# Optimization experiments

Measured on AMD Instinct MI355X. Metric: run time of the kernel, lower is better.

## Reference

```python
import jax, jax.numpy as jnp
import numpy as np

L, H, C, V, T_BLK = 12, 12, 768, 50257, 1024
D = C // H  # head dim = 64


def _layernorm(x, g, b, eps=1e-5):
    m = jnp.mean(x, axis=-1, keepdims=True)
    v = jnp.mean(jnp.square(x - m), axis=-1, keepdims=True)
    return (x - m) * jax.lax.rsqrt(v + eps) * g + b


def setup_inputs() -> dict:
    key = jax.random.key(0)
    ks = jax.random.split(key, 8)
    B, T = 8, 1024
    s = 0.02
    sp = 0.02 / np.sqrt(2 * L)  # c_proj special init
    return {
        "idx": jax.random.randint(ks[0], (B, T), 0, V, dtype=jnp.int32),
        "wte": jax.random.normal(ks[1], (V, C), jnp.float32) * s,
        "wpe": jax.random.normal(ks[2], (T_BLK, C), jnp.float32) * s,
        "ln1_g": jnp.ones((L, C), jnp.float32),
        "ln1_b": jnp.zeros((L, C), jnp.float32),
        "w_qkv": jax.random.normal(ks[3], (L, C, 3 * C), jnp.float32) * s,
        "b_qkv": jnp.zeros((L, 3 * C), jnp.float32),
        "w_ao": jax.random.normal(ks[4], (L, C, C), jnp.float32) * sp,
        "b_ao": jnp.zeros((L, C), jnp.float32),
        "ln2_g": jnp.ones((L, C), jnp.float32),
        "ln2_b": jnp.zeros((L, C), jnp.float32),
        "w_fc": jax.random.normal(ks[5], (L, C, 4 * C), jnp.float32) * s,
        "b_fc": jnp.zeros((L, 4 * C), jnp.float32),
        "w_mo": jax.random.normal(ks[6], (L, 4 * C, C), jnp.float32) * sp,
        "b_mo": jnp.zeros((L, C), jnp.float32),
        "lnf_g": jnp.ones((C,), jnp.float32),
        "lnf_b": jnp.zeros((C,), jnp.float32),
    }


def reference(idx, wte, wpe, ln1_g, ln1_b, w_qkv, b_qkv, w_ao, b_ao,
              ln2_g, ln2_b, w_fc, b_fc, w_mo, b_mo, lnf_g, lnf_b):
    B, T = idx.shape
    scale = 1.0 / np.sqrt(D)
    causal = jnp.tril(jnp.ones((T, T), dtype=bool))  # [T,T]

    x = wte[idx] + wpe[:T]  # [B,T,C]

    def block(x, p):
        g1, b1, wq, bq, wo, bo, g2, b2_, wf, bf, w2, b2m = p
        h = _layernorm(x, g1, b1)
        qkv = h @ wq + bq  # [B,T,3C]
        q, k, v = jnp.split(qkv, 3, axis=-1)
        q = q.reshape(B, T, H, D)
        k = k.reshape(B, T, H, D)
        v = v.reshape(B, T, H, D)
        att = jnp.einsum('bqhd,bkhd->bhqk', q, k) * scale
        att = jnp.where(causal, att, -jnp.inf)
        att = jax.nn.softmax(att, axis=-1)
        y = jnp.einsum('bhqk,bkhd->bqhd', att, v).reshape(B, T, C)
        x = x + y @ wo + bo
        h2 = _layernorm(x, g2, b2_)
        x = x + jax.nn.gelu(h2 @ wf + bf, approximate=False) @ w2 + b2m
        return x, None

    params = (ln1_g, ln1_b, w_qkv, b_qkv, w_ao, b_ao,
              ln2_g, ln2_b, w_fc, b_fc, w_mo, b_mo)
    x, _ = jax.lax.scan(block, x, params)

    x = _layernorm(x, lnf_g, lnf_b)
    # inference path: logits only for last position, lm_head tied to wte
    logits = x[:, -1:, :] @ wte.T  # [B,1,V]
    return logits
```

## Files before the change

kernel.cpp:

```cpp
#include <hip/hip_runtime.h>

#define B_ 8
#define T_ 1024
#define C_ 768
#define H_ 12
#define L_ 12
#define V_ 50257

typedef __bf16 bf16_t;
typedef __bf16 bf16x8 __attribute__((ext_vector_type(8)));
typedef __bf16 bf16x4 __attribute__((ext_vector_type(4)));
typedef float f32x4 __attribute__((ext_vector_type(4)));

#define AS1 __attribute__((address_space(1)))
#define AS3 __attribute__((address_space(3)))

__device__ __forceinline__ unsigned short f2bf(float f) {
  bf16_t h = (bf16_t)f;
  return __builtin_bit_cast(unsigned short, h);
}

__device__ __forceinline__ unsigned short bfbits(bf16_t h) {
  return __builtin_bit_cast(unsigned short, h);
}

template<int CTRL>
__device__ __forceinline__ float dppf(float x) {
  return __builtin_bit_cast(float, __builtin_amdgcn_update_dpp(
      0, __builtin_bit_cast(int, x), CTRL, 0xF, 0xF, true));
}
__device__ __forceinline__ float red16_max(float x) {
  x = fmaxf(x, dppf<0xB1>(x));
  x = fmaxf(x, dppf<0x4E>(x));
  x = fmaxf(x, dppf<0x124>(x));
  x = fmaxf(x, dppf<0x128>(x));
  return x;
}
__device__ __forceinline__ float red16_sum(float x) {
  x += dppf<0xB1>(x);
  x += dppf<0x4E>(x);
  x += dppf<0x124>(x);
  x += dppf<0x128>(x);
  return x;
}

__global__ __launch_bounds__(192) void embed_kernel(
    const int* __restrict__ idx, const float* __restrict__ wte,
    const float* __restrict__ wpe, float* __restrict__ xf)
{
  const int bt = blockIdx.x;
  const int t = bt & (T_ - 1);
  const int tok = idx[bt];
  const int c4 = threadIdx.x << 2;
  float4 a = *(const float4*)(wte + (size_t)tok * C_ + c4);
  float4 p = *(const float4*)(wpe + (size_t)t * C_ + c4);
  float4 r; r.x = a.x + p.x; r.y = a.y + p.y; r.z = a.z + p.z; r.w = a.w + p.w;
  *(float4*)(xf + (size_t)bt * C_ + c4) = r;
}

template<bool LAST>
__global__ __launch_bounds__(256) void ln_kernel(
    const float* __restrict__ x, const float* __restrict__ gw,
    const float* __restrict__ bw, unsigned short* __restrict__ obf,
    float* __restrict__ of)
{
  __shared__ float red[8];
  const size_t row = LAST ? ((size_t)blockIdx.x * T_ + (T_ - 1)) : (size_t)blockIdx.x;
  const float* xr = x + row * C_;
  const int t = threadIdx.x;
  float v0 = xr[t], v1 = xr[t + 256], v2 = xr[t + 512];
  float s = v0 + v1 + v2;
  #pragma unroll
  for (int off = 32; off; off >>= 1) s += __shfl_xor(s, off);
  if ((t & 63) == 0) red[t >> 6] = s;
  __syncthreads();
  const float mean = (red[0] + red[1] + red[2] + red[3]) * (1.0f / C_);
  const float d0 = v0 - mean, d1 = v1 - mean, d2 = v2 - mean;
  float ss = d0 * d0 + d1 * d1 + d2 * d2;
  #pragma unroll
  for (int off = 32; off; off >>= 1) ss += __shfl_xor(ss, off);
  if ((t & 63) == 0) red[4 + (t >> 6)] = ss;
  __syncthreads();
  const float var = (red[4] + red[5] + red[6] + red[7]) * (1.0f / C_);
  const float rs = rsqrtf(var + 1e-5f);
  float o0 = d0 * rs * gw[t] + bw[t];
  float o1 = d1 * rs * gw[t + 256] + bw[t + 256];
  float o2 = d2 * rs * gw[t + 512] + bw[t + 512];
  if (LAST) {
    float* orow = of + (size_t)blockIdx.x * C_;
    orow[t] = o0; orow[t + 256] = o1; orow[t + 512] = o2;
  } else {
    unsigned short* orow = obf + row * C_;
    orow[t] = f2bf(o0); orow[t + 256] = f2bf(o1); orow[t + 512] = f2bf(o2);
  }
}

__global__ __launch_bounds__(256) void cvtw4_kernel(
    const float* __restrict__ wq, const float* __restrict__ wa,
    const float* __restrict__ wf, const float* __restrict__ wm,
    unsigned short* __restrict__ out)
{
  __shared__ float tile[32][33];
  const int i = blockIdx.x;
  const float* W; unsigned short* Wt; int K, N, tix;
  if (i < 1728)      { W = wq; Wt = out;                 K = C_;     N = 3 * C_; tix = i; }
  else if (i < 2304) { W = wa; Wt = out + 3 * C_ * C_;   K = C_;     N = C_;     tix = i - 1728; }
  else if (i < 4608) { W = wf; Wt = out + 4 * C_ * C_;   K = C_;     N = 4 * C_; tix = i - 2304; }
  else               { W = wm; Wt = out + 8 * C_ * C_;   K = 4 * C_; N = C_;     tix = i - 4608; }
  const int ntx = N >> 5;
  const int kb = (tix / ntx) << 5, nb = (tix % ntx) << 5;
  const int t = threadIdx.x;
  {
    const int k = t >> 3, n4 = (t & 7) << 2;
    float4 v = *(const float4*)(W + (size_t)(kb + k) * N + nb + n4);
    tile[k][n4] = v.x; tile[k][n4 + 1] = v.y; tile[k][n4 + 2] = v.z; tile[k][n4 + 3] = v.w;
  }
  __syncthreads();
  {
    const int n = t >> 3, k4 = (t & 7) << 2;
    ushort4 o;
    o.x = f2bf(tile[k4][n]);     o.y = f2bf(tile[k4 + 1][n]);
    o.z = f2bf(tile[k4 + 2][n]); o.w = f2bf(tile[k4 + 3][n]);
    *(ushort4*)(Wt + (size_t)(nb + n) * K + kb + k4) = o;
  }
}

template<int EPI>
__global__ __launch_bounds__(256, 2) void gemm_bt(
    const unsigned short* __restrict__ A, const unsigned short* __restrict__ Bt,
    const float* __restrict__ bias, float* __restrict__ Cf,
    unsigned short* __restrict__ Cb, int M, int N, int K, int nx)
{
  (void)M; (void)nx;
  __shared__ unsigned short As[2][128 * 64];
  __shared__ unsigned short Bs[2][128 * 64];
  const int tid = threadIdx.x;
  const int lane = tid & 63;
  const int w = tid >> 6;
  const int wr = w >> 1, wc = w & 1;
  const int l15 = lane & 15, l4 = lane >> 4;
  const int swz = lane & 7;

  const int bid = blockIdx.x;
  const int xcd = bid & 7;
  const int j = bid >> 3;
  const int mblk = xcd * 8 + (j & 7);
  const int nblk = j >> 3;
  const int m0 = mblk * 128, n0 = nblk * 128;

  f32x4 acc[4][4] = {};

  const int srow = lane >> 3;
  const int schunk = (lane & 7) ^ srow;
  const unsigned short* aSrc = A + (size_t)(m0 + w * 32 + srow) * K + schunk * 8;
  const unsigned short* bSrc = Bt + (size_t)(n0 + w * 32 + srow) * K + schunk * 8;
  const int ldsRowBase = (w * 32) * 64;

  auto stage = [&](int kt, int p) {
    const int k0 = kt << 6;
    #pragma unroll
    for (int jj = 0; jj < 4; ++jj)
      __builtin_amdgcn_global_load_lds(
          (const AS1 unsigned int*)(aSrc + (size_t)jj * 8 * K + k0),
          (AS3 unsigned int*)(&As[p][ldsRowBase + jj * 8 * 64]), 16, 0, 0);
    #pragma unroll
    for (int jj = 0; jj < 4; ++jj)
      __builtin_amdgcn_global_load_lds(
          (const AS1 unsigned int*)(bSrc + (size_t)jj * 8 * K + k0),
          (AS3 unsigned int*)(&Bs[p][ldsRowBase + jj * 8 * 64]), 16, 0, 0);
  };

  auto compute = [&](int p) {
    const unsigned short* aw = &As[p][(wr * 64) * 64];
    const unsigned short* bw2 = &Bs[p][(wc * 64) * 64];
    #pragma unroll
    for (int ks = 0; ks < 2; ++ks) {
      bf16x8 af[4], bf[4];
      #pragma unroll
      for (int mf = 0; mf < 4; ++mf)
        af[mf] = *(const bf16x8*)(aw + (mf * 16 + l15) * 64 + (((ks << 2) | l4) ^ swz) * 8);
      #pragma unroll
      for (int nf = 0; nf < 4; ++nf)
        bf[nf] = *(const bf16x8*)(bw2 + (nf * 16 + l15) * 64 + (((ks << 2) | l4) ^ swz) * 8);
      __builtin_amdgcn_s_setprio(1);
      #pragma unroll
      for (int mf = 0; mf < 4; ++mf)
        #pragma unroll
        for (int nf = 0; nf < 4; ++nf)
          acc[mf][nf] = __builtin_amdgcn_mfma_f32_16x16x32_bf16(af[mf], bf[nf], acc[mf][nf], 0, 0, 0);
      __builtin_amdgcn_s_setprio(0);
    }
  };

  const int nk = K >> 6;
  stage(0, 0);
  for (int kt = 0; kt < nk - 1; ++kt) {
    const int p = kt & 1;
    stage(kt + 1, p ^ 1);
    asm volatile("s_waitcnt vmcnt(8)" ::: "memory");
    __builtin_amdgcn_s_barrier();
    compute(p);
    __builtin_amdgcn_s_barrier();
  }
  asm volatile("s_waitcnt vmcnt(0)" ::: "memory");
  __builtin_amdgcn_s_barrier();
  compute((nk - 1) & 1);

  #pragma unroll
  for (int mf = 0; mf < 4; ++mf) {
    #pragma unroll
    for (int nf = 0; nf < 4; ++nf) {
      const int col = n0 + wc * 64 + nf * 16 + l15;
      const float bv = bias[col];
      int hh = 0, dd = 0;
      unsigned short* qkvo = nullptr;
      if constexpr (EPI == 3) {
        const int which = col / C_;
        const int rem = col - which * C_;
        hh = rem >> 6; dd = rem & 63;
        qkvo = Cb + (size_t)which * ((size_t)B_ * H_ * T_ * 64);
      }
      #pragma unroll
      for (int i = 0; i < 4; ++i) {
        const int row = m0 + wr * 64 + mf * 16 + l4 * 4 + i;
        float v = acc[mf][nf][i] + bv;
        if constexpr (EPI == 1) {
          Cf[(size_t)row * N + col] += v;
        } else if constexpr (EPI == 2) {
          float g = 0.5f * v * (1.0f + erff(v * 0.70710678118f));
          Cb[(size_t)row * N + col] = f2bf(g);
        } else {
          const int bb = row >> 10, tt = row & (T_ - 1);
          qkvo[(((size_t)bb * H_ + hh) * T_ + tt) * 64 + dd] = f2bf(v);
        }
      }
    }
  }
}

__global__ __launch_bounds__(256) void attn_kernel(
    const unsigned short* __restrict__ Qb, const unsigned short* __restrict__ Kb,
    const unsigned short* __restrict__ Vb, unsigned short* __restrict__ y)
{
  const int pb = blockIdx.x / 96;
  const int bh = blockIdx.x % 96;
  const int h = bh % H_;
  const int b = bh / H_;
  const int tid = threadIdx.x, lane = tid & 63, w = tid >> 6;
  const int l15 = lane & 15, l4 = lane >> 4;

  const int qw = (w < 2) ? (pb * 64 + w * 32) : ((15 - pb) * 64 + (w - 2) * 32);
  const int NT = (17 - pb) >> 1;

  __shared__ unsigned short Ks[128 * 64];
  __shared__ unsigned short Vt[64 * 136];
  __shared__ unsigned short Pb[4][32 * 74];

  const unsigned short* qp = Qb + ((size_t)bh * T_ + qw) * 64;
  bf16x8 qf[2][2];
  #pragma unroll
  for (int mf = 0; mf < 2; ++mf)
    #pragma unroll
    for (int ks = 0; ks < 2; ++ks)
      qf[mf][ks] = *(const bf16x8*)(qp + (mf * 16 + l15) * 64 + ks * 32 + l4 * 8);

  f32x4 o[2][4] = {};
  float mrow[2][4], lrow[2][4];
  #pragma unroll
  for (int mf = 0; mf < 2; ++mf)
    #pragma unroll
    for (int i = 0; i < 4; ++i) { mrow[mf][i] = -1e30f; lrow[mf][i] = 0.0f; }

  const unsigned short* kb0 = Kb + (size_t)bh * T_ * 64;
  const unsigned short* vb0 = Vb + (size_t)bh * T_ * 64;
  const int ck = w;
  const int skey = lane;
  const int sw = (skey & 7);

  bf16x8 kr0, kr1, kr2, kr3, vr0, vr1, vr2, vr3;
  {
    const unsigned short* kp = kb0 + (size_t)skey * 64;
    const unsigned short* vp = vb0 + (size_t)skey * 64;
    kr0 = *(const bf16x8*)(kp + ck * 8);
    kr1 = *(const bf16x8*)(kp + (ck + 4) * 8);
    kr2 = *(const bf16x8*)(kp + 64 * 64 + ck * 8);
    kr3 = *(const bf16x8*)(kp + 64 * 64 + (ck + 4) * 8);
    vr0 = *(const bf16x8*)(vp + ck * 8);
    vr1 = *(const bf16x8*)(vp + (ck + 4) * 8);
    vr2 = *(const bf16x8*)(vp + 64 * 64 + ck * 8);
    vr3 = *(const bf16x8*)(vp + 64 * 64 + (ck + 4) * 8);
  }

  for (int kt = 0; kt < NT; ++kt) {
    const int k0 = kt << 7;
    __syncthreads();
    *(bf16x8*)(Ks + skey * 64 + ((ck ^ sw) * 8)) = kr0;
    *(bf16x8*)(Ks + skey * 64 + (((ck + 4) ^ sw) * 8)) = kr1;
    *(bf16x8*)(Ks + (skey + 64) * 64 + ((ck ^ sw) * 8)) = kr2;
    *(bf16x8*)(Ks + (skey + 64) * 64 + (((ck + 4) ^ sw) * 8)) = kr3;
    #pragma unroll
    for (int jj = 0; jj < 8; ++jj) {
      Vt[(ck * 8 + jj) * 136 + skey]            = bfbits(vr0[jj]);
      Vt[((ck + 4) * 8 + jj) * 136 + skey]      = bfbits(vr1[jj]);
      Vt[(ck * 8 + jj) * 136 + skey + 64]       = bfbits(vr2[jj]);
      Vt[((ck + 4) * 8 + jj) * 136 + skey + 64] = bfbits(vr3[jj]);
    }
    __syncthreads();
    if (kt + 1 < NT) {
      const int kn = (kt + 1) << 7;
      const unsigned short* kp = kb0 + (size_t)(kn + skey) * 64;
      const unsigned short* vp = vb0 + (size_t)(kn + skey) * 64;
      kr0 = *(const bf16x8*)(kp + ck * 8);
      kr1 = *(const bf16x8*)(kp + (ck + 4) * 8);
      kr2 = *(const bf16x8*)(kp + 64 * 64 + ck * 8);
      kr3 = *(const bf16x8*)(kp + 64 * 64 + (ck + 4) * 8);
      vr0 = *(const bf16x8*)(vp + ck * 8);
      vr1 = *(const bf16x8*)(vp + (ck + 4) * 8);
      vr2 = *(const bf16x8*)(vp + 64 * 64 + ck * 8);
      vr3 = *(const bf16x8*)(vp + 64 * 64 + (ck + 4) * 8);
    }

    #pragma unroll
    for (int h2 = 0; h2 < 2; ++h2) {
      const int kh0 = k0 + h2 * 64;
      if (kh0 > qw + 31) continue;

      f32x4 s[2][4] = {};
      __builtin_amdgcn_s_setprio(1);
      #pragma unroll
      for (int ks = 0; ks < 2; ++ks) {
        #pragma unroll
        for (int nfk = 0; nfk < 4; ++nfk) {
          const int key = h2 * 64 + nfk * 16 + l15;
          bf16x8 kf = *(const bf16x8*)(Ks + key * 64 + ((((ks << 2) | l4) ^ (l15 & 7)) * 8));
          #pragma unroll
          for (int mf = 0; mf < 2; ++mf)
            s[mf][nfk] = __builtin_amdgcn_mfma_f32_16x16x32_bf16(qf[mf][ks], kf, s[mf][nfk], 0, 0, 0);
        }
      }
      __builtin_amdgcn_s_setprio(0);

      #pragma unroll
      for (int mf = 0; mf < 2; ++mf) {
        const int qrow = qw + mf * 16 + l4 * 4;
        const bool fullt = (kh0 + 63) <= (qw + mf * 16);
        float pvv[4][4], tm[4];
        #pragma unroll
        for (int i = 0; i < 4; ++i) {
          const int q = qrow + i;
          float m_ = -1e30f;
          #pragma unroll
          for (int nfk = 0; nfk < 4; ++nfk) {
            float x = s[mf][nfk][i] * 0.125f;
            x = fullt ? x : ((kh0 + nfk * 16 + l15 <= q) ? x : -1e30f);
            pvv[nfk][i] = x;
            m_ = fmaxf(m_, x);
          }
          tm[i] = red16_max(m_);
        }
        bool need = false;
        #pragma unroll
        for (int i = 0; i < 4; ++i) need |= (tm[i] > mrow[mf][i] + 8.0f);
        if (__any(need)) {
          #pragma unroll
          for (int i = 0; i < 4; ++i) {
            const float mnew = fmaxf(mrow[mf][i], tm[i]);
            const float alpha = __expf(mrow[mf][i] - mnew);
            mrow[mf][i] = mnew;
            lrow[mf][i] *= alpha;
            #pragma unroll
            for (int nf = 0; nf < 4; ++nf) o[mf][nf][i] *= alpha;
          }
        }
        #pragma unroll
        for (int i = 0; i < 4; ++i) {
          float rsum = 0.0f;
          #pragma unroll
          for (int nfk = 0; nfk < 4; ++nfk) {
            const float p = __expf(pvv[nfk][i] - mrow[mf][i]);
            pvv[nfk][i] = p; rsum += p;
          }
          rsum = red16_sum(rsum);
          lrow[mf][i] += rsum;
        }
        #pragma unroll
        for (int nfk = 0; nfk < 4; ++nfk)
          #pragma unroll
          for (int i = 0; i < 4; ++i)
            Pb[w][(mf * 16 + l4 * 4 + i) * 74 + nfk * 16 + l15] = f2bf(pvv[nfk][i]);
      }

      bf16x8 pa[2][2];
      #pragma unroll
      for (int mf = 0; mf < 2; ++mf)
        #pragma unroll
        for (int k2 = 0; k2 < 2; ++k2)
          pa[mf][k2] = *(const bf16x8*)(Pb[w] + (mf * 16 + l15) * 74 + k2 * 32 + l4 * 8);
      __builtin_amdgcn_s_setprio(1);
      #pragma unroll
      for (int nf = 0; nf < 4; ++nf) {
        const int d = nf * 16 + l15;
        #pragma unroll
        for (int k2 = 0; k2 < 2; ++k2) {
          bf16x8 vf = *(const bf16x8*)(Vt + d * 136 + h2 * 64 + k2 * 32 + l4 * 8);
          #pragma unroll
          for (int mf = 0; mf < 2; ++mf)
            o[mf][nf] = __builtin_amdgcn_mfma_f32_16x16x32_bf16(pa[mf][k2], vf, o[mf][nf], 0, 0, 0);
        }
      }
      __builtin_amdgcn_s_setprio(0);
    }
  }

  #pragma unroll
  for (int mf = 0; mf < 2; ++mf) {
    #pragma unroll
    for (int i = 0; i < 4; ++i) {
      const float inv = 1.0f / lrow[mf][i];
      const int q = qw + mf * 16 + l4 * 4 + i;
      unsigned short* yr = y + (size_t)(b * T_ + q) * C_ + h * 64;
      #pragma unroll
      for (int nf = 0; nf < 4; ++nf)
        yr[nf * 16 + l15] = f2bf(o[mf][nf][i] * inv);
    }
  }
}

__global__ __launch_bounds__(256) void head_kernel(
    const float* __restrict__ lnf, const float* __restrict__ wte,
    float* __restrict__ out)
{
  __shared__ float xs[B_ * C_];
  for (int i = threadIdx.x; i < B_ * C_; i += 256) xs[i] = lnf[i];
  __syncthreads();
  const int w = threadIdx.x >> 6, lane = threadIdx.x & 63;
  const int v = blockIdx.x * 4 + w;
  if (v >= V_) return;
  const float* wv = wte + (size_t)v * C_ + lane * 12;
  float4 w0 = *(const float4*)(wv);
  float4 w1 = *(const float4*)(wv + 4);
  float4 w2 = *(const float4*)(wv + 8);
  float acc[B_];
  #pragma unroll
  for (int bb = 0; bb < B_; ++bb) {
    const float* xr = xs + bb * C_ + lane * 12;
    float4 x0 = *(const float4*)(xr);
    float4 x1 = *(const float4*)(xr + 4);
    float4 x2 = *(const float4*)(xr + 8);
    acc[bb] = w0.x * x0.x + w0.y * x0.y + w0.z * x0.z + w0.w * x0.w
            + w1.x * x1.x + w1.y * x1.y + w1.z * x1.z + w1.w * x1.w
            + w2.x * x2.x + w2.y * x2.y + w2.z * x2.z + w2.w * x2.w;
  }
  #pragma unroll
  for (int off = 32; off; off >>= 1) {
    #pragma unroll
    for (int bb = 0; bb < B_; ++bb)
      acc[bb] += __shfl_xor(acc[bb], off);
  }
  if (lane == 0) {
    #pragma unroll
    for (int bb = 0; bb < B_; ++bb)
      out[(size_t)bb * V_ + v] = acc[bb];
  }
}

extern "C" void kernel_launch(void* const* d_in, const int* in_sizes, int n_in,
                              void* d_out, int out_size, void* d_ws, size_t ws_size,
                              hipStream_t stream)
{
  (void)in_sizes; (void)n_in; (void)out_size; (void)ws_size;
  const int*   idx   = (const int*)d_in[0];
  const float* wte   = (const float*)d_in[1];
  const float* wpe   = (const float*)d_in[2];
  const float* ln1_g = (const float*)d_in[3];
  const float* ln1_b = (const float*)d_in[4];
  const float* w_qkv = (const float*)d_in[5];
  const float* b_qkv = (const float*)d_in[6];
  const float* w_ao  = (const float*)d_in[7];
  const float* b_ao  = (const float*)d_in[8];
  const float* ln2_g = (const float*)d_in[9];
  const float* ln2_b = (const float*)d_in[10];
  const float* w_fc  = (const float*)d_in[11];
  const float* b_fc  = (const float*)d_in[12];
  const float* w_mo  = (const float*)d_in[13];
  const float* b_mo  = (const float*)d_in[14];
  const float* lnf_g = (const float*)d_in[15];
  const float* lnf_b = (const float*)d_in[16];

  char* ws = (char*)d_ws;
  size_t off = 0;
  auto wsalloc = [&](size_t bytes) -> void* {
    void* p = ws + off;
    off += (bytes + 255) & ~(size_t)255;
    return p;
  };
  const size_t SZH = (size_t)B_ * H_ * T_ * 64;
  float* xf             = (float*)wsalloc((size_t)B_ * T_ * C_ * 4);
  unsigned short* qkv3  = (unsigned short*)wsalloc(3 * SZH * 2);
  unsigned short* a_in  = (unsigned short*)wsalloc((size_t)B_ * T_ * C_ * 2);
  unsigned short* act2  = (unsigned short*)wsalloc((size_t)B_ * T_ * 4 * C_ * 2);
  unsigned short* wbuf  = (unsigned short*)wsalloc((size_t)12 * C_ * C_ * 2);
  float* lnfb           = (float*)wsalloc((size_t)B_ * C_ * 4);

  const size_t OFF_AO = (size_t)3 * C_ * C_;
  const size_t OFF_FC = (size_t)4 * C_ * C_;
  const size_t OFF_MO = (size_t)8 * C_ * C_;
  const int MROWS = B_ * T_;

  embed_kernel<<<B_ * T_, 192, 0, stream>>>(idx, wte, wpe, xf);

  for (int l = 0; l < L_; ++l) {
    ln_kernel<false><<<B_ * T_, 256, 0, stream>>>(xf, ln1_g + l * C_, ln1_b + l * C_, a_in, nullptr);
    cvtw4_kernel<<<6912, 256, 0, stream>>>(
        w_qkv + (size_t)l * C_ * 3 * C_, w_ao + (size_t)l * C_ * C_,
        w_fc + (size_t)l * C_ * 4 * C_, w_mo + (size_t)l * 4 * C_ * C_, wbuf);
    gemm_bt<3><<<64 * 18, 256, 0, stream>>>(a_in, wbuf, b_qkv + l * 3 * C_, nullptr, qkv3, MROWS, 3 * C_, C_, 18);
    attn_kernel<<<8 * B_ * H_, 256, 0, stream>>>(qkv3, qkv3 + SZH, qkv3 + 2 * SZH, a_in);
    gemm_bt<1><<<64 * 6, 256, 0, stream>>>(a_in, wbuf + OFF_AO, b_ao + l * C_, xf, nullptr, MROWS, C_, C_, 6);
    ln_kernel<false><<<B_ * T_, 256, 0, stream>>>(xf, ln2_g + l * C_, ln2_b + l * C_, a_in, nullptr);
    gemm_bt<2><<<64 * 24, 256, 0, stream>>>(a_in, wbuf + OFF_FC, b_fc + l * 4 * C_, nullptr, act2, MROWS, 4 * C_, C_, 24);
    gemm_bt<1><<<64 * 6, 256, 0, stream>>>(act2, wbuf + OFF_MO, b_mo + l * C_, xf, nullptr, MROWS, C_, 4 * C_, 6);
  }

  ln_kernel<true><<<B_, 256, 0, stream>>>(xf, lnf_g, lnf_b, nullptr, lnfb);
  head_kernel<<<(V_ + 3) / 4, 256, 0, stream>>>(lnfb, wte, (float*)d_out);
}
```

Baseline: 3.713 ms.

## Add 256x256-tile 8-wave GEMM kernel for QKV and FC projections

Adds a new gemm256 kernel that uses 512 threads and 256x256 output tiles, splitting the tile into four quadrant sub-steps per K-tile. Each sub-step interleaves the prefetch of one half-tile into double-buffered LDS with MFMA work. The QKV and FC GEMMs now use this kernel, which raises arithmetic intensity per LDS byte and reduces the number of blocks. The attention-output and MLP-out GEMMs keep the older kernel, whose tile mapping changes from fixed 8-wide groups to division by nx. The trade-off is one block per CU, higher register use, many barriers per K-step, and fewer blocks (288/384), which may leave the machine underfilled.

```diff
diff --git a/kernel.cpp b/kernel.cpp
--- a/kernel.cpp
+++ b/kernel.cpp
@@ -126,88 +126,138 @@
 }
 
 template<int EPI>
-__global__ __launch_bounds__(256, 2) void gemm_bt(
+__global__ __launch_bounds__(512, 1) void gemm256(
     const unsigned short* __restrict__ A, const unsigned short* __restrict__ Bt,
-    const float* __restrict__ bias, float* __restrict__ Cf,
-    unsigned short* __restrict__ Cb, int M, int N, int K, int nx)
-{
-  (void)M; (void)nx;
-  __shared__ unsigned short As[2][128 * 64];
-  __shared__ unsigned short Bs[2][128 * 64];
+    const float* __restrict__ bias, unsigned short* __restrict__ Cb,
+    int N, int K, int nx)
+{
+  __shared__ __align__(16) unsigned short As[2][2][128 * 64];
+  __shared__ __align__(16) unsigned short Bs[2][2][128 * 64];
   const int tid = threadIdx.x;
   const int lane = tid & 63;
   const int w = tid >> 6;
-  const int wr = w >> 1, wc = w & 1;
+  const int wr = w >> 2;
+  const int wc = w & 3;
   const int l15 = lane & 15, l4 = lane >> 4;
-  const int swz = lane & 7;
+  const int s7 = l15 & 7;
 
   const int bid = blockIdx.x;
   const int xcd = bid & 7;
   const int j = bid >> 3;
-  const int mblk = xcd * 8 + (j & 7);
-  const int nblk = j >> 3;
-  const int m0 = mblk * 128, n0 = nblk * 128;
-
-  f32x4 acc[4][4] = {};
-
-  const int srow = lane >> 3;
-  const int schunk = (lane & 7) ^ srow;
-  const unsigned short* aSrc = A + (size_t)(m0 + w * 32 + srow) * K + schunk * 8;
-  const unsigned short* bSrc = Bt + (size_t)(n0 + w * 32 + srow) * K + schunk * 8;
-  const int ldsRowBase = (w * 32) * 64;
-
-  auto stage = [&](int kt, int p) {
-    const int k0 = kt << 6;
-    #pragma unroll
-    for (int jj = 0; jj < 4; ++jj)
+  const int mblk = xcd * 4 + j / nx;
+  const int nblk = j - (j / nx) * nx;
+  const int m0 = mblk * 256, n0 = nblk * 256;
+
+  f32x4 acc[8][4] = {};
+
+  const int srow8 = lane >> 3;
+  const int sch = (lane & 7) ^ srow8;
+
+  auto stageA = [&](int h, int kt, int q) {
+    const size_t k0 = (size_t)kt * 64;
+    #pragma unroll
+    for (int jj = 0; jj < 2; ++jj)
       __builtin_amdgcn_global_load_lds(
-          (const AS1 unsigned int*)(aSrc + (size_t)jj * 8 * K + k0),
-          (AS3 unsigned int*)(&As[p][ldsRowBase + jj * 8 * 64]), 16, 0, 0);
-    #pragma unroll
-    for (int jj = 0; jj < 4; ++jj)
+          (const AS1 unsigned int*)(A + (size_t)(m0 + h * 128 + jj * 64 + w * 8 + srow8) * K + sch * 8 + k0),
+          (AS3 unsigned int*)(&As[q][h][(jj * 8 + w) * 512]), 16, 0, 0);
+  };
+  auto stageB = [&](int h, int kt, int q) {
+    const size_t k0 = (size_t)kt * 64;
+    #pragma unroll
+    for (int jj = 0; jj < 2; ++jj)
       __builtin_amdgcn_global_load_lds(
-          (const AS1 unsigned int*)(bSrc + (size_t)jj * 8 * K + k0),
-          (AS3 unsigned int*)(&Bs[p][ldsRowBase + jj * 8 * 64]), 16, 0, 0);
+          (const AS1 unsigned int*)(Bt + (size_t)(n0 + h * 128 + jj * 64 + w * 8 + srow8) * K + sch * 8 + k0),
+          (AS3 unsigned int*)(&Bs[q][h][(jj * 8 + w) * 512]), 16, 0, 0);
   };
 
-  auto compute = [&](int p) {
-    const unsigned short* aw = &As[p][(wr * 64) * 64];
-    const unsigned short* bw2 = &Bs[p][(wc * 64) * 64];
-    #pragma unroll
-    for (int ks = 0; ks < 2; ++ks) {
-      bf16x8 af[4], bf[4];
-      #pragma unroll
-      for (int mf = 0; mf < 4; ++mf)
-        af[mf] = *(const bf16x8*)(aw + (mf * 16 + l15) * 64 + (((ks << 2) | l4) ^ swz) * 8);
-      #pragma unroll
-      for (int nf = 0; nf < 4; ++nf)
-        bf[nf] = *(const bf16x8*)(bw2 + (nf * 16 + l15) * 64 + (((ks << 2) | l4) ^ swz) * 8);
-      __builtin_amdgcn_s_setprio(1);
-      #pragma unroll
-      for (int mf = 0; mf < 4; ++mf)
-        #pragma unroll
-        for (int nf = 0; nf < 4; ++nf)
-          acc[mf][nf] = __builtin_amdgcn_mfma_f32_16x16x32_bf16(af[mf], bf[nf], acc[mf][nf], 0, 0, 0);
-      __builtin_amdgcn_s_setprio(0);
-    }
-  };
-
   const int nk = K >> 6;
-  stage(0, 0);
-  for (int kt = 0; kt < nk - 1; ++kt) {
-    const int p = kt & 1;
-    stage(kt + 1, p ^ 1);
-    asm volatile("s_waitcnt vmcnt(8)" ::: "memory");
-    __builtin_amdgcn_s_barrier();
-    compute(p);
-    __builtin_amdgcn_s_barrier();
-  }
-  asm volatile("s_waitcnt vmcnt(0)" ::: "memory");
-  __builtin_amdgcn_s_barrier();
-  compute((nk - 1) & 1);
-
-  #pragma unroll
-  for (int mf = 0; mf < 4; ++mf) {
+  stageA(0, 0, 0); stageA(1, 0, 0); stageB(0, 0, 0); stageB(1, 0, 0);
+
+  for (int t = 0; t < nk; ++t) {
+    const int p = t & 1, q = p ^ 1;
+    const bool pf = (t + 1 < nk);
+    bf16x8 Af[4][2], Bf[2][2];
+    auto rdA = [&](int f, int ks) -> bf16x8 {
+      return *(const bf16x8*)(&As[p][wr][(f * 16 + l15) * 64 + ((((ks << 2) | l4) ^ s7) << 3)]);
+    };
+    auto rdB = [&](int nf, int ks) -> bf16x8 {
+      return *(const bf16x8*)(&Bs[p][wc >> 1][((wc & 1) * 64 + nf * 16 + l15) * 64 + ((((ks << 2) | l4) ^ s7) << 3)]);
+    };
+
+    if (pf) { stageA(0, t + 1, q); asm volatile("s_waitcnt vmcnt(2)" ::: "memory"); }
+    else    { asm volatile("s_waitcnt vmcnt(0)" ::: "memory"); }
+    __builtin_amdgcn_s_barrier();
+    #pragma unroll
+    for (int f = 0; f < 4; ++f) { Af[f][0] = rdA(f, 0); Af[f][1] = rdA(f, 1); }
+    #pragma unroll
+    for (int nf = 0; nf < 2; ++nf) { Bf[nf][0] = rdB(nf, 0); Bf[nf][1] = rdB(nf, 1); }
+    asm volatile("s_waitcnt lgkmcnt(0)" ::: "memory");
+    __builtin_amdgcn_sched_barrier(0);
+    __builtin_amdgcn_s_setprio(1);
+    #pragma unroll
+    for (int f = 0; f < 4; ++f)
+      #pragma unroll
+      for (int nf = 0; nf < 2; ++nf)
+        #pragma unroll
+        for (int ks = 0; ks < 2; ++ks)
+          acc[f][nf] = __builtin_amdgcn_mfma_f32_16x16x32_bf16(Af[f][ks], Bf[nf][ks], acc[f][nf], 0, 0, 0);
+    __builtin_amdgcn_s_setprio(0);
+    __builtin_amdgcn_s_barrier();
+
+    if (pf) stageA(1, t + 1, q);
+    #pragma unroll
+    for (int nf = 0; nf < 2; ++nf) { Bf[nf][0] = rdB(nf + 2, 0); Bf[nf][1] = rdB(nf + 2, 1); }
+    __builtin_amdgcn_s_barrier();
+    asm volatile("s_waitcnt lgkmcnt(0)" ::: "memory");
+    __builtin_amdgcn_sched_barrier(0);
+    __builtin_amdgcn_s_setprio(1);
+    #pragma unroll
+    for (int f = 0; f < 4; ++f)
+      #pragma unroll
+      for (int nf = 0; nf < 2; ++nf)
+        #pragma unroll
+        for (int ks = 0; ks < 2; ++ks)
+          acc[f][nf + 2] = __builtin_amdgcn_mfma_f32_16x16x32_bf16(Af[f][ks], Bf[nf][ks], acc[f][nf + 2], 0, 0, 0);
+    __builtin_amdgcn_s_setprio(0);
+    __builtin_amdgcn_s_barrier();
+
+    if (pf) stageB(0, t + 1, q);
+    #pragma unroll
+    for (int f = 0; f < 4; ++f) { Af[f][0] = rdA(f + 4, 0); Af[f][1] = rdA(f + 4, 1); }
+    __builtin_amdgcn_s_barrier();
+    asm volatile("s_waitcnt lgkmcnt(0)" ::: "memory");
+    __builtin_amdgcn_sched_barrier(0);
+    __builtin_amdgcn_s_setprio(1);
+    #pragma unroll
+    for (int f = 0; f < 4; ++f)
+      #pragma unroll
+      for (int nf = 0; nf < 2; ++nf)
+        #pragma unroll
+        for (int ks = 0; ks < 2; ++ks)
+          acc[f + 4][nf + 2] = __builtin_amdgcn_mfma_f32_16x16x32_bf16(Af[f][ks], Bf[nf][ks], acc[f + 4][nf + 2], 0, 0, 0);
+    __builtin_amdgcn_s_setprio(0);
+    __builtin_amdgcn_s_barrier();
+
+    if (pf) stageB(1, t + 1, q);
+    #pragma unroll
+    for (int nf = 0; nf < 2; ++nf) { Bf[nf][0] = rdB(nf, 0); Bf[nf][1] = rdB(nf, 1); }
+    __builtin_amdgcn_s_barrier();
+    asm volatile("s_waitcnt lgkmcnt(0)" ::: "memory");
+    __builtin_amdgcn_sched_barrier(0);
+    __builtin_amdgcn_s_setprio(1);
+    #pragma unroll
+    for (int f = 0; f < 4; ++f)
+      #pragma unroll
+      for (int nf = 0; nf < 2; ++nf)
+        #pragma unroll
+        for (int ks = 0; ks < 2; ++ks)
+          acc[f + 4][nf] = __builtin_amdgcn_mfma_f32_16x16x32_bf16(Af[f][ks], Bf[nf][ks], acc[f + 4][nf], 0, 0, 0);
+    __builtin_amdgcn_s_setprio(0);
+    __builtin_amdgcn_s_barrier();
+  }
+
+  #pragma unroll
+  for (int f = 0; f < 8; ++f) {
     #pragma unroll
     for (int nf = 0; nf < 4; ++nf) {
       const int col = n0 + wc * 64 + nf * 16 + l15;
@@ -222,6 +272,109 @@
       }
       #pragma unroll
       for (int i = 0; i < 4; ++i) {
+        const int row = mblk * 256 + wr * 128 + f * 16 + l4 * 4 + i;
+        float v = acc[f][nf][i] + bv;
+        if constexpr (EPI == 2) {
+          float g = 0.5f * v * (1.0f + erff(v * 0.70710678118f));
+          Cb[(size_t)row * N + col] = f2bf(g);
+        } else {
+          const int bb = row >> 10, tt = row & (T_ - 1);
+          qkvo[(((size_t)bb * H_ + hh) * T_ + tt) * 64 + dd] = f2bf(v);
+        }
+      }
+    }
+  }
+}
+
+template<int EPI>
+__global__ __launch_bounds__(256, 2) void gemm_bt(
+    const unsigned short* __restrict__ A, const unsigned short* __restrict__ Bt,
+    const float* __restrict__ bias, float* __restrict__ Cf,
+    unsigned short* __restrict__ Cb, int M, int N, int K, int nx)
+{
+  (void)M;
+  __shared__ unsigned short As[2][128 * 64];
+  __shared__ unsigned short Bs[2][128 * 64];
+  const int tid = threadIdx.x;
+  const int lane = tid & 63;
+  const int w = tid >> 6;
+  const int wr = w >> 1, wc = w & 1;
+  const int l15 = lane & 15, l4 = lane >> 4;
+  const int swz = lane & 7;
+
+  const int bid = blockIdx.x;
+  const int xcd = bid & 7;
+  const int j = bid >> 3;
+  const int mblk = xcd * 8 + j / nx;
+  const int nblk = j - (j / nx) * nx;
+  const int m0 = mblk * 128, n0 = nblk * 128;
+
+  f32x4 acc[4][4] = {};
+
+  const int srow = lane >> 3;
+  const int schunk = (lane & 7) ^ srow;
+  const unsigned short* aSrc = A + (size_t)(m0 + w * 32 + srow) * K + schunk * 8;
+  const unsigned short* bSrc = Bt + (size_t)(n0 + w * 32 + srow) * K + schunk * 8;
+  const int ldsRowBase = (w * 32) * 64;
+
+  auto stage = [&](int kt, int p) {
+    const int k0 = kt << 6;
+    #pragma unroll
+    for (int jj = 0; jj < 4; ++jj)
+      __builtin_amdgcn_global_load_lds(
+          (const AS1 unsigned int*)(aSrc + (size_t)jj * 8 * K + k0),
+          (AS3 unsigned int*)(&As[p][ldsRowBase + jj * 8 * 64]), 16, 0, 0);
+    #pragma unroll
+    for (int jj = 0; jj < 4; ++jj)
+      __builtin_amdgcn_global_load_lds(
+          (const AS1 unsigned int*)(bSrc + (size_t)jj * 8 * K + k0),
+          (AS3 unsigned int*)(&Bs[p][ldsRowBase + jj * 8 * 64]), 16, 0, 0);
+  };
+
+  auto compute = [&](int p) {
+    const unsigned short* aw = &As[p][(wr * 64) * 64];
+    const unsigned short* bw2 = &Bs[p][(wc * 64) * 64];
+    #pragma unroll
+    for (int ks = 0; ks < 2; ++ks) {
+      bf16x8 af[4], bf[4];
+      #pragma unroll
+      for (int mf = 0; mf < 4; ++mf)
+        af[mf] = *(const bf16x8*)(aw + (mf * 16 + l15) * 64 + (((ks << 2) | l4) ^ swz) * 8);
+      #pragma unroll
+      for (int nf = 0; nf < 4; ++nf)
+        bf[nf] = *(const bf16x8*)(bw2 + (nf * 16 + l15) * 64 + (((ks << 2) | l4) ^ swz) * 8);
+      __builtin_amdgcn_s_setprio(1);
+      #pragma unroll
+      for (int mf = 0; mf < 4; ++mf)
+        #pragma unroll
+        for (int nf = 0; nf < 4; ++nf)
+          acc[mf][nf] = __builtin_amdgcn_mfma_f32_16x16x32_bf16(af[mf], bf[nf], acc[mf][nf], 0, 0, 0);
+      __builtin_amdgcn_s_setprio(0);
+    }
+  };
+
+  const int nk = K >> 6;
+  stage(0, 0);
+  for (int kt = 0; kt < nk - 1; ++kt) {
+    const int p = kt & 1;
+    stage(kt + 1, p ^ 1);
+    asm volatile("s_waitcnt vmcnt(8)" ::: "memory");
+    __builtin_amdgcn_s_barrier();
+    compute(p);
+    __builtin_amdgcn_s_barrier();
+  }
+  asm volatile("s_waitcnt vmcnt(0)" ::: "memory");
+  __builtin_amdgcn_s_barrier();
+  compute((nk - 1) & 1);
+
+  #pragma unroll
+  for (int mf = 0; mf < 4; ++mf) {
+    #pragma unroll
+    for (int nf = 0; nf < 4; ++nf) {
+      const int col = n0 + wc * 64 + nf * 16 + l15;
+      const float bv = bias[col];
+      #pragma unroll
+      for (int i = 0; i < 4; ++i) {
         const int row = m0 + wr * 64 + mf * 16 + l4 * 4 + i;
         float v = acc[mf][nf][i] + bv;
         if constexpr (EPI == 1) {
@@ -229,9 +382,6 @@
         } else if constexpr (EPI == 2) {
           float g = 0.5f * v * (1.0f + erff(v * 0.70710678118f));
           Cb[(size_t)row * N + col] = f2bf(g);
-        } else {
-          const int bb = row >> 10, tt = row & (T_ - 1);
-          qkvo[(((size_t)bb * H_ + hh) * T_ + tt) * 64 + dd] = f2bf(v);
         }
       }
     }
@@ -514,11 +664,11 @@
     cvtw4_kernel<<<6912, 256, 0, stream>>>(
         w_qkv + (size_t)l * C_ * 3 * C_, w_ao + (size_t)l * C_ * C_,
         w_fc + (size_t)l * C_ * 4 * C_, w_mo + (size_t)l * 4 * C_ * C_, wbuf);
-    gemm_bt<3><<<64 * 18, 256, 0, stream>>>(a_in, wbuf, b_qkv + l * 3 * C_, nullptr, qkv3, MROWS, 3 * C_, C_, 18);
+    gemm256<3><<<288, 512, 0, stream>>>(a_in, wbuf, b_qkv + l * 3 * C_, qkv3, 3 * C_, C_, 9);
     attn_kernel<<<8 * B_ * H_, 256, 0, stream>>>(qkv3, qkv3 + SZH, qkv3 + 2 * SZH, a_in);
     gemm_bt<1><<<64 * 6, 256, 0, stream>>>(a_in, wbuf + OFF_AO, b_ao + l * C_, xf, nullptr, MROWS, C_, C_, 6);
     ln_kernel<false><<<B_ * T_, 256, 0, stream>>>(xf, ln2_g + l * C_, ln2_b + l * C_, a_in, nullptr);
-    gemm_bt<2><<<64 * 24, 256, 0, stream>>>(a_in, wbuf + OFF_FC, b_fc + l * 4 * C_, nullptr, act2, MROWS, 4 * C_, C_, 24);
+    gemm256<2><<<384, 512, 0, stream>>>(a_in, wbuf + OFF_FC, b_fc + l * 4 * C_, act2, 4 * C_, C_, 12);
     gemm_bt<1><<<64 * 6, 256, 0, stream>>>(act2, wbuf + OFF_MO, b_mo + l * C_, xf, nullptr, MROWS, C_, 4 * C_, 6);
   }
 
```

Result: slower. 4.404 ms (+18.6%).

## Halve GEMM K-tile to raise occupancy, remap block grid, use polynomial GELU

Applied to the files above, without the earlier changes.

The GEMM K-step drops from 64 to 32. This halves shared memory per block, and launch bounds now target 4 blocks per CU instead of 2, for more latency hiding. The LDS swizzle and wait counts are adjusted to match, and the block-to-tile mapping now uses the nx parameter instead of a hard-coded 8. The exact erff in the GELU epilogue is replaced with the Abramowitz-Stegun polynomial using __expf, which cuts epilogue cost at some loss of accuracy. The cost is twice as many barriers per K and a tighter register budget that could spill.

```diff
diff --git a/kernel.cpp b/kernel.cpp
--- a/kernel.cpp
+++ b/kernel.cpp
@@ -22,6 +22,20 @@
 
 __device__ __forceinline__ unsigned short bfbits(bf16_t h) {
   return __builtin_bit_cast(unsigned short, h);
+}
+
+__device__ __forceinline__ float fast_gelu(float v) {
+  const float xe = v * 0.70710678118f;
+  const float ax = fabsf(xe);
+  const float t = 1.0f / fmaf(0.3275911f, ax, 1.0f);
+  float poly = fmaf(t, 1.061405429f, -1.453152027f);
+  poly = fmaf(t, poly, 1.421413741f);
+  poly = fmaf(t, poly, -0.284496736f);
+  poly = fmaf(t, poly, 0.254829592f);
+  poly *= t;
+  float er = 1.0f - poly * __expf(-ax * ax);
+  er = (xe < 0.0f) ? -er : er;
+  return 0.5f * v * (1.0f + er);
 }
 
 template<int CTRL>
@@ -126,78 +140,74 @@
 }
 
 template<int EPI>
-__global__ __launch_bounds__(256, 2) void gemm_bt(
+__global__ __launch_bounds__(256, 4) void gemm_bt(
     const unsigned short* __restrict__ A, const unsigned short* __restrict__ Bt,
     const float* __restrict__ bias, float* __restrict__ Cf,
     unsigned short* __restrict__ Cb, int M, int N, int K, int nx)
 {
-  (void)M; (void)nx;
-  __shared__ unsigned short As[2][128 * 64];
-  __shared__ unsigned short Bs[2][128 * 64];
+  (void)M;
+  __shared__ unsigned short As[2][128 * 32];
+  __shared__ unsigned short Bs[2][128 * 32];
   const int tid = threadIdx.x;
   const int lane = tid & 63;
   const int w = tid >> 6;
   const int wr = w >> 1, wc = w & 1;
   const int l15 = lane & 15, l4 = lane >> 4;
-  const int swz = lane & 7;
 
   const int bid = blockIdx.x;
   const int xcd = bid & 7;
   const int j = bid >> 3;
-  const int mblk = xcd * 8 + (j & 7);
-  const int nblk = j >> 3;
+  const int mblk = xcd * 8 + j / nx;
+  const int nblk = j - (j / nx) * nx;
   const int m0 = mblk * 128, n0 = nblk * 128;
 
   f32x4 acc[4][4] = {};
 
-  const int srow = lane >> 3;
-  const int schunk = (lane & 7) ^ srow;
-  const unsigned short* aSrc = A + (size_t)(m0 + w * 32 + srow) * K + schunk * 8;
+  const int srow = lane >> 2;
+  const int schunk = (lane & 3) ^ (srow & 3);
+  const unsigned short* aSrc = A  + (size_t)(m0 + w * 32 + srow) * K + schunk * 8;
   const unsigned short* bSrc = Bt + (size_t)(n0 + w * 32 + srow) * K + schunk * 8;
-  const int ldsRowBase = (w * 32) * 64;
+  const int ldsBase = (w * 32) * 32;
 
   auto stage = [&](int kt, int p) {
-    const int k0 = kt << 6;
-    #pragma unroll
-    for (int jj = 0; jj < 4; ++jj)
+    const int k0 = kt << 5;
+    #pragma unroll
+    for (int jj = 0; jj < 2; ++jj)
       __builtin_amdgcn_global_load_lds(
-          (const AS1 unsigned int*)(aSrc + (size_t)jj * 8 * K + k0),
-          (AS3 unsigned int*)(&As[p][ldsRowBase + jj * 8 * 64]), 16, 0, 0);
-    #pragma unroll
-    for (int jj = 0; jj < 4; ++jj)
+          (const AS1 unsigned int*)(aSrc + (size_t)jj * 16 * K + k0),
+          (AS3 unsigned int*)(&As[p][ldsBase + jj * 16 * 32]), 16, 0, 0);
+    #pragma unroll
+    for (int jj = 0; jj < 2; ++jj)
       __builtin_amdgcn_global_load_lds(
-          (const AS1 unsigned int*)(bSrc + (size_t)jj * 8 * K + k0),
-          (AS3 unsigned int*)(&Bs[p][ldsRowBase + jj * 8 * 64]), 16, 0, 0);
+          (const AS1 unsigned int*)(bSrc + (size_t)jj * 16 * K + k0),
+          (AS3 unsigned int*)(&Bs[p][ldsBase + jj * 16 * 32]), 16, 0, 0);
   };
 
   auto compute = [&](int p) {
-    const unsigned short* aw = &As[p][(wr * 64) * 64];
-    const unsigned short* bw2 = &Bs[p][(wc * 64) * 64];
-    #pragma unroll
-    for (int ks = 0; ks < 2; ++ks) {
-      bf16x8 af[4], bf[4];
-      #pragma unroll
-      for (int mf = 0; mf < 4; ++mf)
-        af[mf] = *(const bf16x8*)(aw + (mf * 16 + l15) * 64 + (((ks << 2) | l4) ^ swz) * 8);
+    const unsigned short* aw  = &As[p][(wr * 64) * 32];
+    const unsigned short* bw2 = &Bs[p][(wc * 64) * 32];
+    bf16x8 af[4], bf[4];
+    #pragma unroll
+    for (int mf = 0; mf < 4; ++mf)
+      af[mf] = *(const bf16x8*)(aw + (mf * 16 + l15) * 32 + ((l4 ^ (l15 & 3)) << 3));
+    #pragma unroll
+    for (int nf = 0; nf < 4; ++nf)
+      bf[nf] = *(const bf16x8*)(bw2 + (nf * 16 + l15) * 32 + ((l4 ^ (l15 & 3)) << 3));
+    __builtin_amdgcn_s_setprio(1);
+    #pragma unroll
+    for (int mf = 0; mf < 4; ++mf)
       #pragma unroll
       for (int nf = 0; nf < 4; ++nf)
-        bf[nf] = *(const bf16x8*)(bw2 + (nf * 16 + l15) * 64 + (((ks << 2) | l4) ^ swz) * 8);
-      __builtin_amdgcn_s_setprio(1);
-      #pragma unroll
-      for (int mf = 0; mf < 4; ++mf)
-        #pragma unroll
-        for (int nf = 0; nf < 4; ++nf)
-          acc[mf][nf] = __builtin_amdgcn_mfma_f32_16x16x32_bf16(af[mf], bf[nf], acc[mf][nf], 0, 0, 0);
-      __builtin_amdgcn_s_setprio(0);
-    }
+        acc[mf][nf] = __builtin_amdgcn_mfma_f32_16x16x32_bf16(af[mf], bf[nf], acc[mf][nf], 0, 0, 0);
+    __builtin_amdgcn_s_setprio(0);
   };
 
-  const int nk = K >> 6;
+  const int nk = K >> 5;
   stage(0, 0);
   for (int kt = 0; kt < nk - 1; ++kt) {
     const int p = kt & 1;
     stage(kt + 1, p ^ 1);
-    asm volatile("s_waitcnt vmcnt(8)" ::: "memory");
+    asm volatile("s_waitcnt vmcnt(4)" ::: "memory");
     __builtin_amdgcn_s_barrier();
     compute(p);
     __builtin_amdgcn_s_barrier();
@@ -227,8 +237,7 @@
         if constexpr (EPI == 1) {
           Cf[(size_t)row * N + col] += v;
         } else if constexpr (EPI == 2) {
-          float g = 0.5f * v * (1.0f + erff(v * 0.70710678118f));
-          Cb[(size_t)row * N + col] = f2bf(g);
+          Cb[(size_t)row * N + col] = f2bf(fast_gelu(v));
         } else {
           const int bb = row >> 10, tt = row & (T_ - 1);
           qkvo[(((size_t)bb * H_ + hh) * T_ + tt) * 64 + dd] = f2bf(v);
```

After: 3.942 ms. 6.2% more time.

## Interleave causal query bands per wave and use a fast GELU approximation

Applied to the files above, without the earlier changes.

Each wave in the attention kernel now owns one 16-row query band from the early tile and one from the late tile, instead of one wave pair owning 32 rows from a single tile. Every wave therefore sees a similar amount of causal work, and the MFMAs and softmax for an inactive band are skipped per key half. Separately, the GELU epilogue replaces erff with the Abramowitz-Stegun polynomial erf approximation using __expf, which is cheaper but less accurate. The extra branching and the lower GELU precision are the costs.

```diff
diff --git a/kernel.cpp b/kernel.cpp
--- a/kernel.cpp
+++ b/kernel.cpp
@@ -22,6 +22,20 @@
 
 __device__ __forceinline__ unsigned short bfbits(bf16_t h) {
   return __builtin_bit_cast(unsigned short, h);
+}
+
+__device__ __forceinline__ float fast_gelu(float v) {
+  const float xe = v * 0.70710678118f;
+  const float ax = fabsf(xe);
+  const float t = 1.0f / fmaf(0.3275911f, ax, 1.0f);
+  float poly = fmaf(t, 1.061405429f, -1.453152027f);
+  poly = fmaf(t, poly, 1.421413741f);
+  poly = fmaf(t, poly, -0.284496736f);
+  poly = fmaf(t, poly, 0.254829592f);
+  poly *= t;
+  float er = 1.0f - poly * __expf(-ax * ax);
+  er = (xe < 0.0f) ? -er : er;
+  return 0.5f * v * (1.0f + er);
 }
 
 template<int CTRL>
@@ -227,8 +241,7 @@
         if constexpr (EPI == 1) {
           Cf[(size_t)row * N + col] += v;
         } else if constexpr (EPI == 2) {
-          float g = 0.5f * v * (1.0f + erff(v * 0.70710678118f));
-          Cb[(size_t)row * N + col] = f2bf(g);
+          Cb[(size_t)row * N + col] = f2bf(fast_gelu(v));
         } else {
           const int bb = row >> 10, tt = row & (T_ - 1);
           qkvo[(((size_t)bb * H_ + hh) * T_ + tt) * 64 + dd] = f2bf(v);
@@ -249,20 +262,24 @@
   const int tid = threadIdx.x, lane = tid & 63, w = tid >> 6;
   const int l15 = lane & 15, l4 = lane >> 4;
 
-  const int qw = (w < 2) ? (pb * 64 + w * 32) : ((15 - pb) * 64 + (w - 2) * 32);
+  const int qband0 = pb * 64 + w * 16;
+  const int qband1 = (15 - pb) * 64 + w * 16;
   const int NT = (17 - pb) >> 1;
 
   __shared__ unsigned short Ks[128 * 64];
   __shared__ unsigned short Vt[64 * 136];
   __shared__ unsigned short Pb[4][32 * 74];
 
-  const unsigned short* qp = Qb + ((size_t)bh * T_ + qw) * 64;
   bf16x8 qf[2][2];
-  #pragma unroll
-  for (int mf = 0; mf < 2; ++mf)
-    #pragma unroll
-    for (int ks = 0; ks < 2; ++ks)
-      qf[mf][ks] = *(const bf16x8*)(qp + (mf * 16 + l15) * 64 + ks * 32 + l4 * 8);
+  {
+    const unsigned short* q0p = Qb + ((size_t)bh * T_ + qband0) * 64;
+    const unsigned short* q1p = Qb + ((size_t)bh * T_ + qband1) * 64;
+    #pragma unroll
+    for (int ks = 0; ks < 2; ++ks) {
+      qf[0][ks] = *(const bf16x8*)(q0p + l15 * 64 + ks * 32 + l4 * 8);
+      qf[1][ks] = *(const bf16x8*)(q1p + l15 * 64 + ks * 32 + l4 * 8);
+    }
+  }
 
   f32x4 o[2][4] = {};
   float mrow[2][4], lrow[2][4];
@@ -323,7 +340,9 @@
     #pragma unroll
     for (int h2 = 0; h2 < 2; ++h2) {
       const int kh0 = k0 + h2 * 64;
-      if (kh0 > qw + 31) continue;
+      const bool act0 = (kh0 <= qband0 + 15);
+      const bool act1 = (kh0 <= qband1 + 15);
+      if (!act0 && !act1) continue;
 
       f32x4 s[2][4] = {};
       __builtin_amdgcn_s_setprio(1);
@@ -333,17 +352,19 @@
         for (int nfk = 0; nfk < 4; ++nfk) {
           const int key = h2 * 64 + nfk * 16 + l15;
           bf16x8 kf = *(const bf16x8*)(Ks + key * 64 + ((((ks << 2) | l4) ^ (l15 & 7)) * 8));
-          #pragma unroll
-          for (int mf = 0; mf < 2; ++mf)
-            s[mf][nfk] = __builtin_amdgcn_mfma_f32_16x16x32_bf16(qf[mf][ks], kf, s[mf][nfk], 0, 0, 0);
+          if (act0) s[0][nfk] = __builtin_amdgcn_mfma_f32_16x16x32_bf16(qf[0][ks], kf, s[0][nfk], 0, 0, 0);
+          if (act1) s[1][nfk] = __builtin_amdgcn_mfma_f32_16x16x32_bf16(qf[1][ks], kf, s[1][nfk], 0, 0, 0);
         }
       }
       __builtin_amdgcn_s_setprio(0);
 
       #pragma unroll
       for (int mf = 0; mf < 2; ++mf) {
-        const int qrow = qw + mf * 16 + l4 * 4;
-        const bool fullt = (kh0 + 63) <= (qw + mf * 16);
+        const bool act = mf ? act1 : act0;
+        if (!act) continue;
+        const int qb0 = mf ? qband1 : qband0;
+        const int qrow = qb0 + l4 * 4;
+        const bool fullt = (kh0 + 63) <= qb0;
         float pvv[4][4], tm[4];
         #pragma unroll
         for (int i = 0; i < 4; ++i) {
@@ -393,9 +414,10 @@
       bf16x8 pa[2][2];
       #pragma unroll
       for (int mf = 0; mf < 2; ++mf)
-        #pragma unroll
-        for (int k2 = 0; k2 < 2; ++k2)
-          pa[mf][k2] = *(const bf16x8*)(Pb[w] + (mf * 16 + l15) * 74 + k2 * 32 + l4 * 8);
+        if (mf ? act1 : act0)
+          #pragma unroll
+          for (int k2 = 0; k2 < 2; ++k2)
+            pa[mf][k2] = *(const bf16x8*)(Pb[w] + (mf * 16 + l15) * 74 + k2 * 32 + l4 * 8);
       __builtin_amdgcn_s_setprio(1);
       #pragma unroll
       for (int nf = 0; nf < 4; ++nf) {
@@ -403,9 +425,8 @@
         #pragma unroll
         for (int k2 = 0; k2 < 2; ++k2) {
           bf16x8 vf = *(const bf16x8*)(Vt + d * 136 + h2 * 64 + k2 * 32 + l4 * 8);
-          #pragma unroll
-          for (int mf = 0; mf < 2; ++mf)
-            o[mf][nf] = __builtin_amdgcn_mfma_f32_16x16x32_bf16(pa[mf][k2], vf, o[mf][nf], 0, 0, 0);
+          if (act0) o[0][nf] = __builtin_amdgcn_mfma_f32_16x16x32_bf16(pa[0][k2], vf, o[0][nf], 0, 0, 0);
+          if (act1) o[1][nf] = __builtin_amdgcn_mfma_f32_16x16x32_bf16(pa[1][k2], vf, o[1][nf], 0, 0, 0);
         }
       }
       __builtin_amdgcn_s_setprio(0);
@@ -414,10 +435,11 @@
 
   #pragma unroll
   for (int mf = 0; mf < 2; ++mf) {
+    const int qb0 = mf ? qband1 : qband0;
     #pragma unroll
     for (int i = 0; i < 4; ++i) {
       const float inv = 1.0f / lrow[mf][i];
-      const int q = qw + mf * 16 + l4 * 4 + i;
+      const int q = qb0 + l4 * 4 + i;
       unsigned short* yr = y + (size_t)(b * T_ + q) * C_ + h * 64;
       #pragma unroll
       for (int nf = 0; nf < 4; ++nf)
```

Result: no change. 3.659 ms (-1.4%).
